# Optimization experiments

Hardware: AMD Instinct MI355X
Metric: run time of the kernel (lower is better)

## Reference

```python
import jax, jax.numpy as jnp
import numpy as np

N = 8192
F_DIM = 512
H_DIM = 256


def _xavier(key, shape):
    fan_in, fan_out = shape
    limit = float(np.sqrt(6.0 / (fan_in + fan_out)))
    return jax.random.uniform(key, shape, jnp.float32, -limit, limit)


def setup_inputs() -> dict:
    key = jax.random.key(0)
    k1, k2, k3, k4, k5, k6, k7 = jax.random.split(key, 7)
    inp = {
        "input": jax.random.normal(k1, (N, F_DIM), jnp.float32),
        "wavelets": jax.random.normal(k2, (N, N), jnp.float32) / np.sqrt(N),
        "wavelets_inv": jax.random.normal(k3, (N, N), jnp.float32) / np.sqrt(N),
        "W1": _xavier(k4, (F_DIM, H_DIM)),
        "W2": _xavier(k5, (H_DIM, H_DIM)),
        "filter1": jax.random.uniform(k6, (N,), jnp.float32, 0.9, 1.1),
        "filter2": jax.random.uniform(k7, (N,), jnp.float32, 0.9, 1.1),
    }
    return inp


def _gwnn_layer(x, wavelets, wavelets_inv, weight, filt):
    # torch: wavelets @ diag(filt) @ (wavelets_inv @ (x @ W))
    # diag(filt) right-multiply == column-wise scale of wavelets (same math,
    # avoids the O(N^3) dense diag matmul).
    t = x @ weight                      # [N, C_out]
    s = wavelets_inv @ t                # [N, C_out] (spectral domain)
    return (wavelets * filt[None, :]) @ s  # [N, C_out]


def reference(input, wavelets, wavelets_inv, W1, W2, filter1, filter2):
    # eval mode: dropout is identity
    h1 = jax.nn.relu(_gwnn_layer(input, wavelets, wavelets_inv, W1, filter1))
    out = _gwnn_layer(h1, wavelets, wavelets_inv, W2, filter2)
    return out
```

## Files before the change

### kernel.cpp

```cpp
#include <hip/hip_runtime.h>
#include <hip/hip_bf16.h>

using f32x4 = __attribute__((ext_vector_type(4))) float;
using s16x8 = __attribute__((ext_vector_type(8))) short;

#define DEVFN static __device__ __forceinline__

static constexpr int NCOL = 256;
static constexpr int MROWS = 8192;
static constexpr int BM = 64;
static constexpr int BK = 64;
static constexpr int THREADS = 512;
static constexpr int NTILE = MROWS / BM;
static constexpr size_t PSLICE = (size_t)MROWS * NCOL;

DEVFN unsigned short f2bf(float f) {
  union { float f; unsigned u; } x; x.f = f;
  unsigned u = x.u;
  u += 0x7fffu + ((u >> 16) & 1u);
  return (unsigned short)(u >> 16);
}

DEVFN float bf2f(unsigned short u) {
  union { unsigned u; float f; } x; x.u = (unsigned)u << 16; return x.f;
}

DEVFN s16x8 pack8(f32x4 v0, f32x4 v1) {
  union { s16x8 v; __hip_bfloat162 h[4]; } pk;
  pk.h[0] = __float22bfloat162_rn(float2{v0[0], v0[1]});
  pk.h[1] = __float22bfloat162_rn(float2{v0[2], v0[3]});
  pk.h[2] = __float22bfloat162_rn(float2{v1[0], v1[1]});
  pk.h[3] = __float22bfloat162_rn(float2{v1[2], v1[3]});
  return pk.v;
}

DEVFN void async16(void* lds, const void* g) {
  __builtin_amdgcn_global_load_lds((const __attribute__((address_space(1))) unsigned*)g,
                                   (__attribute__((address_space(3))) unsigned*)lds,
                                   16, 0, 0);
}


template<bool AF32, bool WB, int KS>
__global__ __launch_bounds__(THREADS, 4)
void gemm_f(const void* __restrict__ Aany, int Kfull,
            const unsigned short* __restrict__ Bp8,
            unsigned short* __restrict__ Pout,
            unsigned short* __restrict__ Awb)
{
  __shared__ __align__(16) unsigned short As[2][4096];
  __shared__ __align__(16) unsigned short Bs[2][16384];

  const int nwg = NTILE * KS, q = nwg / 8;
  const int logical = (blockIdx.x & 7) * q + (blockIdx.x >> 3);
  const int kh = logical / NTILE;
  const int tile = logical % NTILE;
  const int klen = Kfull / KS;
  const int nt = klen / BK;
  const int k0 = kh * klen;
  const int KT = Kfull >> 6;
  const int kt0 = k0 >> 6;
  const int tid = threadIdx.x, lane = tid & 63;
  const int wm = (tid >> 6) >> 2;
  const int wn = (tid >> 6) & 3;
  const int lr = lane & 15, lg = lane >> 4;
  const int srow = tid >> 3, sk8 = tid & 7;

  auto stageB = [&](int buf, int t) {
    const unsigned short* b = Bp8 + (size_t)(k0 + t * BK) * 256 + tid * 8;
#pragma unroll
    for (int o = 0; o < 4; ++o)
      async16(&Bs[buf][o * 4096 + tid * 8], b + o * 4096);
  };
  auto stageA_bf = [&](int buf, int t) {
    async16(&As[buf][tid * 8],
            (const unsigned short*)Aany + ((size_t)tile * KT + kt0 + t) * 4096 + tid * 8);
  };

  f32x4 ra0, ra1;
  auto loadA = [&](int t) {
    const float* p = (const float*)Aany + (size_t)(tile * BM + srow) * Kfull
                   + k0 + t * BK + sk8 * 8;
    ra0 = *(const f32x4*)p; ra1 = *(const f32x4*)(p + 4);
  };
  auto putA = [&](int buf, int t) {
    s16x8 v = pack8(ra0, ra1);
    *(s16x8*)&As[buf][sk8 * 512 + srow * 8] = v;
    if constexpr (WB)
      *(s16x8*)&Awb[((size_t)tile * KT + kt0 + t) * 4096 + sk8 * 512 + srow * 8] = v;
  };

  f32x4 acc[2][4] = {};

  if constexpr (AF32) {
    loadA(0); stageB(0, 0); putA(0, 0);
    asm volatile("s_waitcnt lgkmcnt(0)");
  } else {
    stageA_bf(0, 0); stageB(0, 0);
  }

  int cur = 0;
  for (int t = 0; t < nt; ++t) {
    if constexpr (AF32) {
      if (t + 1 < nt) {
        loadA(t + 1);
        stageB(cur ^ 1, t + 1);
        if constexpr (WB) asm volatile("s_waitcnt vmcnt(7)");
        else              asm volatile("s_waitcnt vmcnt(6)");
      } else {
        asm volatile("s_waitcnt vmcnt(0)");
      }
    } else {
      if (t + 1 < nt) {
        stageA_bf(cur ^ 1, t + 1); stageB(cur ^ 1, t + 1);
        asm volatile("s_waitcnt vmcnt(5)");
      } else {
        asm volatile("s_waitcnt vmcnt(0)");
      }
    }
    __builtin_amdgcn_s_barrier();
    __builtin_amdgcn_sched_barrier(0);
    __builtin_amdgcn_s_setprio(1);
#pragma unroll
    for (int s = 0; s < 2; ++s) {
      const int kc = s * 4 + lg;
      s16x8 a0 = *(const s16x8*)&As[cur][kc * 512 + (wm * 32 + lr) * 8];
      s16x8 a1 = *(const s16x8*)&As[cur][kc * 512 + (wm * 32 + 16 + lr) * 8];
#pragma unroll
      for (int fn = 0; fn < 4; ++fn) {
        s16x8 b = *(const s16x8*)&Bs[cur][kc * 2048 + (wn * 64 + fn * 16 + lr) * 8];
        acc[0][fn] = __builtin_amdgcn_mfma_f32_16x16x32_bf16(a0, b, acc[0][fn], 0, 0, 0);
        acc[1][fn] = __builtin_amdgcn_mfma_f32_16x16x32_bf16(a1, b, acc[1][fn], 0, 0, 0);
      }
    }
    __builtin_amdgcn_s_setprio(0);
    if constexpr (AF32) {
      __builtin_amdgcn_sched_barrier(0);
      if (t + 1 < nt) putA(cur ^ 1, t + 1);
      asm volatile("s_waitcnt lgkmcnt(0)");
      __builtin_amdgcn_sched_barrier(0);
    }
    __builtin_amdgcn_s_barrier();
    cur ^= 1;
  }

  unsigned short* dst = Pout + (size_t)kh * PSLICE;
#pragma unroll
  for (int fm = 0; fm < 2; ++fm) {
    const int r0 = tile * BM + wm * 32 + fm * 16 + lg * 4;
#pragma unroll
    for (int fn = 0; fn < 4; ++fn) {
      const int col = wn * 64 + fn * 16 + lr;
      ushort4 u;
      u.x = f2bf(acc[fm][fn][0]); u.y = f2bf(acc[fm][fn][1]);
      u.z = f2bf(acc[fm][fn][2]); u.w = f2bf(acc[fm][fn][3]);
      *(ushort4*)&dst[((size_t)(r0 >> 3) * 256 + col) * 8 + (r0 & 7)] = u;
    }
  }
}


__global__ void k_convert_w(const float* __restrict__ W1, const float* __restrict__ W2,
                            unsigned short* __restrict__ W1p,
                            unsigned short* __restrict__ W2p) {
  const bool is2 = blockIdx.x >= 128;
  const float* W = is2 ? W2 : W1;
  unsigned short* outp = is2 ? W2p : W1p;
  int tid = (is2 ? (blockIdx.x - 128) : blockIdx.x) * blockDim.x + threadIdx.x;
  int j = tid & (NCOL - 1);
  int i0 = (tid >> 8) << 2;
  unsigned short u[4];
#pragma unroll
  for (int r = 0; r < 4; ++r) u[r] = f2bf(W[(size_t)(i0 + r) * NCOL + j]);
  size_t off = ((size_t)(i0 >> 3) * NCOL + j) * 8 + (i0 & 7);
  *(ushort4*)&outp[off] = make_ushort4(u[0], u[1], u[2], u[3]);
}

template<int MODE>
__global__ void k_reduce(const unsigned short* __restrict__ P,
                         const float* __restrict__ filt, void* __restrict__ Out) {
  const int tid = blockIdx.x * blockDim.x + threadIdx.x;
  const int j = tid & 255;
  const int i8 = tid >> 8;
  const int i0 = i8 * 8;
  const size_t base = ((size_t)i8 * 256 + j) * 8;
  float f[8] = {};
#pragma unroll
  for (int h = 0; h < 4; ++h) {
    s16x8 pv = *(const s16x8*)&P[base + (size_t)h * PSLICE];
#pragma unroll
    for (int r = 0; r < 8; ++r) f[r] += bf2f((unsigned short)pv[r]);
  }
  if constexpr (MODE == 0) {
    if (filt) {
#pragma unroll
      for (int r = 0; r < 8; ++r) f[r] *= filt[i0 + r];
    }
    union { s16x8 v; unsigned short u[8]; } o;
#pragma unroll
    for (int r = 0; r < 8; ++r) o.u[r] = f2bf(f[r]);
    *(s16x8*)&((unsigned short*)Out)[base] = o.v;
  } else if constexpr (MODE == 1) {
    unsigned short* O = (unsigned short*)Out;
#pragma unroll
    for (int r = 0; r < 8; ++r) {
      const int row = i0 + r;
      O[((size_t)(row >> 6) * 4 + (j >> 6)) * 4096 + ((j >> 3) & 7) * 512
        + (row & 63) * 8 + (j & 7)] = f2bf(fmaxf(f[r], 0.f));
    }
  } else {
    float* O = (float*)Out;
#pragma unroll
    for (int r = 0; r < 8; ++r)
      O[(size_t)(i0 + r) * NCOL + j] = f[r];
  }
}

extern "C" void kernel_launch(void* const* d_in, const int* in_sizes, int n_in,
                              void* d_out, int out_size, void* d_ws, size_t ws_size,
                              hipStream_t stream) {
  const float* input = (const float*)d_in[0];
  const float* Wv    = (const float*)d_in[1];
  const float* Winv  = (const float*)d_in[2];
  const float* W1    = (const float*)d_in[3];
  const float* W2    = (const float*)d_in[4];
  const float* f1    = (const float*)d_in[5];
  const float* f2    = (const float*)d_in[6];
  float* out = (float*)d_out;

  char* ws = (char*)d_ws;
  unsigned short* WvB   = (unsigned short*)(ws);
  unsigned short* WinvB = (unsigned short*)(ws + 0x8000000);
  unsigned short* partB = (unsigned short*)(ws + 0x10000000);
  unsigned short* t1p   = (unsigned short*)(ws + 0x11000000);
  unsigned short* s1p   = (unsigned short*)(ws + 0x11400000);
  unsigned short* t2p   = (unsigned short*)(ws + 0x11800000);
  unsigned short* s2p   = (unsigned short*)(ws + 0x11C00000);
  unsigned short* h1b   = (unsigned short*)(ws + 0x12000000);
  unsigned short* W1p   = (unsigned short*)(ws + 0x12400000);
  unsigned short* W2p   = (unsigned short*)(ws + 0x12440000);

  dim3 gT(THREADS);
  dim3 g4(NTILE * 4), g1(NTILE);
  dim3 rT(256), rG(MROWS * NCOL / 8 / 256);

  k_convert_w<<<dim3(192), rT, 0, stream>>>(W1, W2, W1p, W2p);

  gemm_f<true, false, 1><<<g1, gT, 0, stream>>>(
      (const void*)input, 512, W1p, t1p, nullptr);
  gemm_f<true, true, 4><<<g4, gT, 0, stream>>>(
      (const void*)Winv, 8192, t1p, partB, WinvB);
  k_reduce<0><<<rG, rT, 0, stream>>>(partB, f1, s1p);
  gemm_f<true, true, 4><<<g4, gT, 0, stream>>>(
      (const void*)Wv, 8192, s1p, partB, WvB);
  k_reduce<1><<<rG, rT, 0, stream>>>(partB, nullptr, h1b);
  gemm_f<false, false, 1><<<g1, gT, 0, stream>>>(
      (const void*)h1b, 256, W2p, t2p, nullptr);
  gemm_f<false, false, 4><<<g4, gT, 0, stream>>>(
      (const void*)WinvB, 8192, t2p, partB, nullptr);
  k_reduce<0><<<rG, rT, 0, stream>>>(partB, f2, s2p);
  gemm_f<false, false, 4><<<g4, gT, 0, stream>>>(
      (const void*)WvB, 8192, s2p, partB, nullptr);
  k_reduce<2><<<rG, rT, 0, stream>>>(partB, nullptr, out);
}
```

Measured before the change: 362.4 us.

## Add per-wave-private bf16 GEMM with split-K 2 for second layer

Adds a new GEMM kernel for the two big second-layer products, which read the already-converted bf16 wavelet matrices. Each of its four waves stages its own A and B tiles into a private LDS region, so the kernel needs no block barriers, and it uses a 64x64 per-wave accumulator tile. Split-K drops from 4 to 2, which halves the partial-sum traffic and the reduce work. The trade-off is fewer workgroups (256) at one block per CU, so parallelism drops, and each wave loads the A tile redundantly into its own region.

```diff
diff --git a/kernel.cpp b/kernel.cpp
--- a/kernel.cpp
+++ b/kernel.cpp
@@ -159,6 +159,88 @@
   }
 }
 
+template<int KS>
+__global__ __launch_bounds__(256, 1)
+void gemm_w(const unsigned short* __restrict__ Ap, int Kfull,
+            const unsigned short* __restrict__ Bp8,
+            unsigned short* __restrict__ Pout)
+{
+  __shared__ __align__(16) unsigned short L[4][2][8192];
+
+  const int nwg = NTILE * KS, q = nwg / 8;
+  const int logical = (blockIdx.x & 7) * q + (blockIdx.x >> 3);
+  const int kh = logical / NTILE;
+  const int tile = logical % NTILE;
+  const int klen = Kfull / KS;
+  const int nt = klen / BK;
+  const int k0 = kh * klen;
+  const int KT = Kfull >> 6;
+  const int kt0 = k0 >> 6;
+  const int tid = threadIdx.x, lane = tid & 63;
+  const int wv = tid >> 6;
+  const int lr = lane & 15, lg = lane >> 4;
+
+  auto stage = [&](int buf, int t) {
+    const unsigned short* a = Ap + ((size_t)tile * KT + kt0 + t) * 4096 + lane * 8;
+#pragma unroll
+    for (int o = 0; o < 8; ++o)
+      async16(&L[wv][buf][o * 512 + lane * 8], a + o * 512);
+    const size_t kg0 = (size_t)(k0 + t * BK) >> 3;
+#pragma unroll
+    for (int g = 0; g < 8; ++g)
+      async16(&L[wv][buf][4096 + g * 512 + lane * 8],
+              Bp8 + ((kg0 + g) * 256 + wv * 64) * 8 + lane * 8);
+  };
+
+  f32x4 acc[4][4] = {};
+
+  stage(0, 0);
+
+  int cur = 0;
+  for (int t = 0; t < nt; ++t) {
+    if (t + 1 < nt) {
+      stage(cur ^ 1, t + 1);
+      asm volatile("s_waitcnt vmcnt(16)");
+    } else {
+      asm volatile("s_waitcnt vmcnt(0)");
+    }
+    __builtin_amdgcn_sched_barrier(0);
+    __builtin_amdgcn_s_setprio(1);
+#pragma unroll
+    for (int s = 0; s < 2; ++s) {
+      const int kc = s * 4 + lg;
+      s16x8 af[4], bf[4];
+#pragma unroll
+      for (int fm = 0; fm < 4; ++fm)
+        af[fm] = *(const s16x8*)&L[wv][cur][kc * 512 + (fm * 16 + lr) * 8];
+#pragma unroll
+      for (int fn = 0; fn < 4; ++fn)
+        bf[fn] = *(const s16x8*)&L[wv][cur][4096 + kc * 512 + (fn * 16 + lr) * 8];
+#pragma unroll
+      for (int fm = 0; fm < 4; ++fm)
+#pragma unroll
+        for (int fn = 0; fn < 4; ++fn)
+          acc[fm][fn] = __builtin_amdgcn_mfma_f32_16x16x32_bf16(af[fm], bf[fn], acc[fm][fn], 0, 0, 0);
+    }
+    __builtin_amdgcn_s_setprio(0);
+    cur ^= 1;
+  }
+
+  unsigned short* dst = Pout + (size_t)kh * PSLICE;
+#pragma unroll
+  for (int fm = 0; fm < 4; ++fm) {
+    const int r0 = tile * BM + fm * 16 + lg * 4;
+#pragma unroll
+    for (int fn = 0; fn < 4; ++fn) {
+      const int col = wv * 64 + fn * 16 + lr;
+      ushort4 u;
+      u.x = f2bf(acc[fm][fn][0]); u.y = f2bf(acc[fm][fn][1]);
+      u.z = f2bf(acc[fm][fn][2]); u.w = f2bf(acc[fm][fn][3]);
+      *(ushort4*)&dst[((size_t)(r0 >> 3) * 256 + col) * 8 + (r0 & 7)] = u;
+    }
+  }
+}
+
 
 __global__ void k_convert_w(const float* __restrict__ W1, const float* __restrict__ W2,
                             unsigned short* __restrict__ W1p,
@@ -176,7 +258,7 @@
   *(ushort4*)&outp[off] = make_ushort4(u[0], u[1], u[2], u[3]);
 }
 
-template<int MODE>
+template<int NS, int MODE>
 __global__ void k_reduce(const unsigned short* __restrict__ P,
                          const float* __restrict__ filt, void* __restrict__ Out) {
   const int tid = blockIdx.x * blockDim.x + threadIdx.x;
@@ -186,7 +268,7 @@
   const size_t base = ((size_t)i8 * 256 + j) * 8;
   float f[8] = {};
 #pragma unroll
-  for (int h = 0; h < 4; ++h) {
+  for (int h = 0; h < NS; ++h) {
     s16x8 pv = *(const s16x8*)&P[base + (size_t)h * PSLICE];
 #pragma unroll
     for (int r = 0; r < 8; ++r) f[r] += bf2f((unsigned short)pv[r]);
@@ -240,8 +322,8 @@
   unsigned short* W1p   = (unsigned short*)(ws + 0x12400000);
   unsigned short* W2p   = (unsigned short*)(ws + 0x12440000);
 
-  dim3 gT(THREADS);
-  dim3 g4(NTILE * 4), g1(NTILE);
+  dim3 gT(THREADS), wT(256);
+  dim3 g4(NTILE * 4), g2(NTILE * 2), g1(NTILE);
   dim3 rT(256), rG(MROWS * NCOL / 8 / 256);
 
   k_convert_w<<<dim3(192), rT, 0, stream>>>(W1, W2, W1p, W2p);
@@ -250,16 +332,14 @@
       (const void*)input, 512, W1p, t1p, nullptr);
   gemm_f<true, true, 4><<<g4, gT, 0, stream>>>(
       (const void*)Winv, 8192, t1p, partB, WinvB);
-  k_reduce<0><<<rG, rT, 0, stream>>>(partB, f1, s1p);
+  k_reduce<4, 0><<<rG, rT, 0, stream>>>(partB, f1, s1p);
   gemm_f<true, true, 4><<<g4, gT, 0, stream>>>(
       (const void*)Wv, 8192, s1p, partB, WvB);
-  k_reduce<1><<<rG, rT, 0, stream>>>(partB, nullptr, h1b);
+  k_reduce<4, 1><<<rG, rT, 0, stream>>>(partB, nullptr, h1b);
   gemm_f<false, false, 1><<<g1, gT, 0, stream>>>(
       (const void*)h1b, 256, W2p, t2p, nullptr);
-  gemm_f<false, false, 4><<<g4, gT, 0, stream>>>(
-      (const void*)WinvB, 8192, t2p, partB, nullptr);
-  k_reduce<0><<<rG, rT, 0, stream>>>(partB, f2, s2p);
-  gemm_f<false, false, 4><<<g4, gT, 0, stream>>>(
-      (const void*)WvB, 8192, s2p, partB, nullptr);
-  k_reduce<2><<<rG, rT, 0, stream>>>(partB, nullptr, out);
-}
+  gemm_w<2><<<g2, wT, 0, stream>>>(WinvB, 8192, t2p, partB);
+  k_reduce<2, 0><<<rG, rT, 0, stream>>>(partB, f2, s2p);
+  gemm_w<2><<<g2, wT, 0, stream>>>(WvB, 8192, s2p, partB);
+  k_reduce<2, 2><<<rG, rT, 0, stream>>>(partB, nullptr, out);
+}
```

After: 371.5 us. 2.5% more time.
